# Kernel optimization log

Measured on AMD Instinct MI355X. Metric: run time of the kernel, lower is better.

## Reference

```python
import jax, jax.numpy as jnp
import numpy as np

KSIZE = 7
CUBIC_A = -0.5


def cubic_contribution(x, a=CUBIC_A):
    ax = jnp.abs(x)
    ax2 = ax * ax
    ax3 = ax * ax2
    cont_01 = ((a + 2) * ax3 - (a + 3) * ax2 + 1) * (ax <= 1).astype(x.dtype)
    cont_12 = (a * ax3 - 5 * a * ax2 + 8 * a * ax - 4 * a) * jnp.logical_and(ax > 1, ax <= 2).astype(x.dtype)
    return cont_01 + cont_12


def projective_grid(H, W, m, eps_x=0.0, eps_y=0.0):
    # Apply 3x3 homography m to pixel centers (x+eps_x, y+eps_y); returns (2, H*W).
    xs = jnp.arange(W, dtype=jnp.float32) + eps_x
    ys = jnp.arange(H, dtype=jnp.float32) + eps_y
    yy, xx = jnp.meshgrid(ys, xs, indexing='ij')
    xx = xx.ravel()
    yy = yy.ravel()
    X = m[0, 0] * xx + m[0, 1] * yy + m[0, 2]
    Y = m[1, 0] * xx + m[1, 1] * yy + m[1, 2]
    Z = m[2, 0] * xx + m[2, 1] * yy + m[2, 2]
    return jnp.stack((X / Z, Y / Z))


def setup_inputs() -> dict:
    key = jax.random.key(0)
    k1, k2 = jax.random.split(key)
    H = W = 1024
    N = H * W
    # near-identity homography (avoids degenerate perspective divide)
    m_inverse = jnp.eye(3, dtype=jnp.float32) + 0.001 * jax.random.normal(k1, (3, 3), dtype=jnp.float32)
    # source-space sampling positions, in-image range
    grid = jax.random.uniform(k2, (2, N), dtype=jnp.float32) * jnp.array([[W - 1.0], [H - 1.0]], dtype=jnp.float32)
    yi = jnp.arange(N, dtype=jnp.int32)
    return {"m_inverse": m_inverse, "grid": grid, "H": H, "W": W, "yi": yi}


def reference(m_inverse, grid, H, W, yi):
    K = KSIZE
    pad = K // 2
    offset = (K % 2) / 2  # 0.5 for odd kernels

    pos = grid + 1 - offset                      # (2, N)
    pos_frac = pos - jnp.floor(pos)              # (2, N)

    pl = projective_grid(H, W, m_inverse, eps_x=-0.5)
    pr = projective_grid(H, W, m_inverse, eps_x=0.5)
    pt = projective_grid(H, W, m_inverse, eps_y=-0.5)
    pb = projective_grid(H, W, m_inverse, eps_y=0.5)

    du = (pb - pt)[:, yi][:, :, None, None]      # (2, N, 1, 1)
    dv = (pr - pl)[:, yi][:, :, None, None]      # (2, N, 1, 1)

    # regularize |du| >= 1
    len_du = jnp.sqrt(du[0] ** 2 + du[1] ** 2)   # (N, 1, 1)
    mask_du = len_du < 1.0
    du = jnp.where(mask_du[None], du / len_du[None], du)
    len_du = jnp.where(mask_du, 1.0, len_du)

    # regularize |dv| >= 1
    len_dv = jnp.sqrt(dv[0] ** 2 + dv[1] ** 2)
    mask_dv = len_dv < 1.0
    dv = jnp.where(mask_dv[None], dv / len_dv[None], dv)
    len_dv = jnp.where(mask_dv, 1.0, len_dv)

    det = du[0] * dv[1] - du[1] * dv[0]          # (N, 1, 1)
    len_du = len_du * det
    len_dv = len_dv * det

    pos_w = jnp.linspace(pad - K + 1, pad, K).astype(jnp.float32) + offset  # (K,)
    pw = pos_frac[:, :, None] - pos_w[None, None, :]                        # (2, N, K)
    pos_wx = pw[0][:, None, :]                   # (N, 1, K)
    pos_wy = pw[1][:, :, None]                   # (N, K, 1)

    pos_wxp = (dv[1] * pos_wx - du[1] * pos_wy) / len_du  # (N, K, K)
    pos_wyp = (du[0] * pos_wy - dv[0] * pos_wx) / len_dv  # (N, K, K)

    x = du[0] * pos_wxp + du[1] * pos_wyp        # (N, K, K)
    y = dv[0] * pos_wxp + dv[1] * pos_wyp        # (N, K, K)

    weight = (cubic_contribution(x) * cubic_contribution(y)).reshape(x.shape[0], -1)  # (N, K*K)
    weight = weight / jnp.sum(weight, axis=-1, keepdims=True)
    return weight
```

## Files before the change

### kernel.cpp

```cpp
#include <hip/hip_runtime.h>

#define K 7
#define KK 49
#define BLK 256

__device__ __forceinline__ float cubic_c(float x) {
    float ax  = __builtin_fabsf(x);
    float ax2 = ax * ax;
    float ax3 = ax2 * ax;
    float c01 =  1.5f * ax3 - 2.5f * ax2 + 1.0f;
    float c12 = -0.5f * ax3 + 2.5f * ax2 - 4.0f * ax + 2.0f;
    return (ax <= 1.0f) ? c01 : ((ax <= 2.0f) ? c12 : 0.0f);
}

__global__ __launch_bounds__(BLK) void kest_kernel(
    const float* __restrict__ m,
    const float* __restrict__ grid,
    const int*   __restrict__ Wp,
    const int*   __restrict__ yi,
    float*       __restrict__ out,
    int N)
{
    __shared__ float sw[KK][BLK + 1];
    __shared__ float srs[BLK];

    const int tid = threadIdx.x;
    const int i   = blockIdx.x * BLK + tid;

    const float m00 = m[0], m01 = m[1], m02 = m[2];
    const float m10 = m[3], m11 = m[4], m12 = m[5];
    const float m20 = m[6], m21 = m[7], m22 = m[8];
    const int   W   = Wp[0];

    if (i < N) {
        const int j = yi[i];
        const float xx = (float)(j % W);
        const float yy = (float)(j / W);

        const float X0 = m00 * xx + m01 * yy + m02;
        const float Y0 = m10 * xx + m11 * yy + m12;
        const float Z0 = m20 * xx + m21 * yy + m22;

        const float izy = 1.0f / (Z0 * Z0 - 0.25f * m21 * m21);
        float du0 = (m01 * Z0 - m21 * X0) * izy;
        float du1 = (m11 * Z0 - m21 * Y0) * izy;
        const float izx = 1.0f / (Z0 * Z0 - 0.25f * m20 * m20);
        float dv0 = (m00 * Z0 - m20 * X0) * izx;
        float dv1 = (m10 * Z0 - m20 * Y0) * izx;

        float len_du = __builtin_sqrtf(du0 * du0 + du1 * du1);
        if (len_du < 1.0f) {
            float r = 1.0f / len_du;
            du0 *= r; du1 *= r;
            len_du = 1.0f;
        }
        float len_dv = __builtin_sqrtf(dv0 * dv0 + dv1 * dv1);
        if (len_dv < 1.0f) {
            float r = 1.0f / len_dv;
            dv0 *= r; dv1 *= r;
            len_dv = 1.0f;
        }

        const float det  = du0 * dv1 - du1 * dv0;
        const float r_du = 1.0f / (len_du * det);
        const float r_dv = 1.0f / (len_dv * det);

        const float px = grid[i]     + 0.5f;
        const float py = grid[N + i] + 0.5f;
        const float fx = px - __builtin_floorf(px);
        const float fy = py - __builtin_floorf(py);

        float wsum = 0.0f;
#pragma unroll
        for (int ky = 0; ky < K; ++ky) {
            const float wyv = fy + 2.5f - (float)ky;
#pragma unroll
            for (int kx = 0; kx < K; ++kx) {
                const float wxv = fx + 2.5f - (float)kx;
                const float a = (dv1 * wxv - du1 * wyv) * r_du;
                const float b = (du0 * wyv - dv0 * wxv) * r_dv;
                const float x = du0 * a + du1 * b;
                const float y = dv0 * a + dv1 * b;
                const float wv = cubic_c(x) * cubic_c(y);
                sw[ky * K + kx][tid] = wv;
                wsum += wv;
            }
        }
        srs[tid] = 1.0f / wsum;
    }
    __syncthreads();

    const long long base  = (long long)blockIdx.x * (BLK * KK);
    const long long limit = (long long)N * KK;
#pragma unroll
    for (int t = 0; t < KK; ++t) {
        const int idx = t * BLK + tid;
        const int p   = idx / KK;
        const int q   = idx - p * KK;
        const long long g = base + idx;
        if (g < limit) out[g] = sw[q][p] * srs[p];
    }
}

extern "C" void kernel_launch(void* const* d_in, const int* in_sizes, int n_in,
                              void* d_out, int out_size, void* d_ws, size_t ws_size,
                              hipStream_t stream) {
    const float* m    = (const float*)d_in[0];
    const float* grid = (const float*)d_in[1];
    const int*   Wp   = (const int*)d_in[3];
    const int*   yi   = (const int*)d_in[4];
    float*       out  = (float*)d_out;
    const int N = in_sizes[4];

    const int blocks = (N + BLK - 1) / BLK;
    kest_kernel<<<blocks, BLK, 0, stream>>>(m, grid, Wp, yi, out, N);
}
```

Measured before the change: 254.7 us.

## Halve LDS staging, vectorize output stores, fold inner transform into 2x2 matrix

Weights are now held in registers and written to a half-sized shared buffer in two rounds of 128 pixels each. Each round is stored to global memory as float4. The per-tap affine transform is precomputed as a 2x2 matrix, so each tap costs two FMAs, and the cubic kernel is rewritten without branches using max/fma. The smaller LDS footprint and the launch-bounds occupancy hint aim to raise occupancy and widen stores. The cost is 49 live registers per thread and an extra barrier round. The float4 tail guard assumes N*KK is divisible by 4.

```diff
diff --git a/kernel.cpp b/kernel.cpp
--- a/kernel.cpp
+++ b/kernel.cpp
@@ -3,17 +3,19 @@
 #define K 7
 #define KK 49
 #define BLK 256
+#define HALF_PIX 128
+#define CHUNK_FLOATS (HALF_PIX * KK)
+#define CHUNK_F4 (CHUNK_FLOATS / 4)
 
 __device__ __forceinline__ float cubic_c(float x) {
-    float ax  = __builtin_fabsf(x);
-    float ax2 = ax * ax;
-    float ax3 = ax2 * ax;
-    float c01 =  1.5f * ax3 - 2.5f * ax2 + 1.0f;
-    float c12 = -0.5f * ax3 + 2.5f * ax2 - 4.0f * ax + 2.0f;
-    return (ax <= 1.0f) ? c01 : ((ax <= 2.0f) ? c12 : 0.0f);
+    float ax = __builtin_fabsf(x);
+    float t2 = __builtin_fmaxf(2.0f - ax, 0.0f);
+    float t1 = __builtin_fmaxf(1.0f - ax, 0.0f);
+    float r  = (t2 * t2) * __builtin_fmaf(0.5f, t2, -0.5f);
+    return __builtin_fmaf(t1 * t1, __builtin_fmaf(-2.0f, t1, 1.0f), r);
 }
 
-__global__ __launch_bounds__(BLK) void kest_kernel(
+__global__ __launch_bounds__(BLK, 5) void kest_kernel(
     const float* __restrict__ m,
     const float* __restrict__ grid,
     const int*   __restrict__ Wp,
@@ -21,18 +23,21 @@
     float*       __restrict__ out,
     int N)
 {
-    __shared__ float sw[KK][BLK + 1];
-    __shared__ float srs[BLK];
+    __shared__ __align__(16) float lds[CHUNK_FLOATS];
 
     const int tid = threadIdx.x;
     const int i   = blockIdx.x * BLK + tid;
+    const bool valid = (i < N);
 
     const float m00 = m[0], m01 = m[1], m02 = m[2];
     const float m10 = m[3], m11 = m[4], m12 = m[5];
     const float m20 = m[6], m21 = m[7], m22 = m[8];
     const int   W   = Wp[0];
 
-    if (i < N) {
+    float w[KK];
+    float rs = 0.0f;
+
+    if (valid) {
         const int j = yi[i];
         const float xx = (float)(j % W);
         const float yy = (float)(j / W);
@@ -65,6 +70,11 @@
         const float r_du = 1.0f / (len_du * det);
         const float r_dv = 1.0f / (len_dv * det);
 
+        const float Axx = du0 * dv1 * r_du - du1 * dv0 * r_dv;
+        const float Axy = du0 * du1 * (r_dv - r_du);
+        const float Ayx = dv0 * dv1 * (r_du - r_dv);
+        const float Ayy = du0 * dv1 * r_dv - du1 * dv0 * r_du;
+
         const float px = grid[i]     + 0.5f;
         const float py = grid[N + i] + 0.5f;
         const float fx = px - __builtin_floorf(px);
@@ -74,31 +84,55 @@
 #pragma unroll
         for (int ky = 0; ky < K; ++ky) {
             const float wyv = fy + 2.5f - (float)ky;
+            const float xk  = Axy * wyv;
+            const float yk  = Ayy * wyv;
 #pragma unroll
             for (int kx = 0; kx < K; ++kx) {
                 const float wxv = fx + 2.5f - (float)kx;
-                const float a = (dv1 * wxv - du1 * wyv) * r_du;
-                const float b = (du0 * wyv - dv0 * wxv) * r_dv;
-                const float x = du0 * a + du1 * b;
-                const float y = dv0 * a + dv1 * b;
+                const float x = __builtin_fmaf(Axx, wxv, xk);
+                const float y = __builtin_fmaf(Ayx, wxv, yk);
                 const float wv = cubic_c(x) * cubic_c(y);
-                sw[ky * K + kx][tid] = wv;
+                w[ky * K + kx] = wv;
                 wsum += wv;
             }
         }
-        srs[tid] = 1.0f / wsum;
+        rs = 1.0f / wsum;
+    }
+
+    const long long blockBaseF = (long long)blockIdx.x * (BLK * KK);
+    const long long limitF4    = ((long long)N * KK) >> 2;
+
+    if (valid && tid < HALF_PIX) {
+        float* p = &lds[tid * KK];
+#pragma unroll
+        for (int q = 0; q < KK; ++q) p[q] = w[q] * rs;
+    }
+    __syncthreads();
+    {
+        const float4* src = (const float4*)lds;
+        float4*       dst = (float4*)(out + blockBaseF);
+        const long long g0 = blockBaseF >> 2;
+#pragma unroll
+        for (int t = tid; t < CHUNK_F4; t += BLK) {
+            if (g0 + t < limitF4) dst[t] = src[t];
+        }
     }
     __syncthreads();
 
-    const long long base  = (long long)blockIdx.x * (BLK * KK);
-    const long long limit = (long long)N * KK;
+    if (valid && tid >= HALF_PIX) {
+        float* p = &lds[(tid - HALF_PIX) * KK];
 #pragma unroll
-    for (int t = 0; t < KK; ++t) {
-        const int idx = t * BLK + tid;
-        const int p   = idx / KK;
-        const int q   = idx - p * KK;
-        const long long g = base + idx;
-        if (g < limit) out[g] = sw[q][p] * srs[p];
+        for (int q = 0; q < KK; ++q) p[q] = w[q] * rs;
+    }
+    __syncthreads();
+    {
+        const float4* src = (const float4*)lds;
+        float4*       dst = (float4*)(out + blockBaseF + CHUNK_FLOATS);
+        const long long g0 = (blockBaseF + CHUNK_FLOATS) >> 2;
+#pragma unroll
+        for (int t = tid; t < CHUNK_F4; t += BLK) {
+            if (g0 + t < limitF4) dst[t] = src[t];
+        }
     }
 }
 
```

New measurement: 217.7 us. -14.5%, faster.

## Split each pixel's 49 weights across four threads with vectorized float4 stores

Applied to the files above, without the earlier changes.

Each pixel's 7x7 weight computation is now spread over four lanes, which reduce the weight sum with shuffles and write normalized weights into a compact LDS tile that is copied out with float4 stores. The per-tap math is collapsed into a precomputed 2x2 linear map, and the cubic kernel is rewritten branch-free using clamped polynomials. W decoding uses shifts when W is a power of two. This raises parallelism and cuts registers per thread, aiming for better occupancy and wider global stores. It costs four times as many blocks and some redundant per-pixel setup on each lane.

```diff
diff --git a/kernel.cpp b/kernel.cpp
--- a/kernel.cpp
+++ b/kernel.cpp
@@ -3,17 +3,20 @@
 #define K 7
 #define KK 49
 #define BLK 256
+#define TPP 4
+#define PPB (BLK / TPP)
+#define NW 13
+#define CHUNK_F4 (PPB * KK / 4)
 
 __device__ __forceinline__ float cubic_c(float x) {
-    float ax  = __builtin_fabsf(x);
-    float ax2 = ax * ax;
-    float ax3 = ax2 * ax;
-    float c01 =  1.5f * ax3 - 2.5f * ax2 + 1.0f;
-    float c12 = -0.5f * ax3 + 2.5f * ax2 - 4.0f * ax + 2.0f;
-    return (ax <= 1.0f) ? c01 : ((ax <= 2.0f) ? c12 : 0.0f);
+    float ax = __builtin_fabsf(x);
+    float t2 = __builtin_fmaxf(2.0f - ax, 0.0f);
+    float t1 = __builtin_fmaxf(1.0f - ax, 0.0f);
+    float r  = (t2 * t2) * __builtin_fmaf(0.5f, t2, -0.5f);
+    return __builtin_fmaf(t1 * t1, __builtin_fmaf(-2.0f, t1, 1.0f), r);
 }
 
-__global__ __launch_bounds__(BLK) void kest_kernel(
+__global__ __launch_bounds__(BLK, 8) void kest_kernel(
     const float* __restrict__ m,
     const float* __restrict__ grid,
     const int*   __restrict__ Wp,
@@ -21,11 +24,12 @@
     float*       __restrict__ out,
     int N)
 {
-    __shared__ float sw[KK][BLK + 1];
-    __shared__ float srs[BLK];
+    __shared__ __align__(16) float lds[PPB * KK];
 
-    const int tid = threadIdx.x;
-    const int i   = blockIdx.x * BLK + tid;
+    const int tid  = threadIdx.x;
+    const int sub  = tid & (TPP - 1);
+    const int pixL = tid >> 2;
+    const int i    = blockIdx.x * PPB + pixL;
 
     const float m00 = m[0], m01 = m[1], m02 = m[2];
     const float m10 = m[3], m11 = m[4], m12 = m[5];
@@ -34,8 +38,16 @@
 
     if (i < N) {
         const int j = yi[i];
-        const float xx = (float)(j % W);
-        const float yy = (float)(j / W);
+        int yyI, xxI;
+        if ((W & (W - 1)) == 0) {
+            yyI = j >> (__ffs(W) - 1);
+            xxI = j & (W - 1);
+        } else {
+            yyI = j / W;
+            xxI = j - yyI * W;
+        }
+        const float xx = (float)xxI;
+        const float yy = (float)yyI;
 
         const float X0 = m00 * xx + m01 * yy + m02;
         const float Y0 = m10 * xx + m11 * yy + m12;
@@ -65,40 +77,54 @@
         const float r_du = 1.0f / (len_du * det);
         const float r_dv = 1.0f / (len_dv * det);
 
-        const float px = grid[i]     + 0.5f;
-        const float py = grid[N + i] + 0.5f;
-        const float fx = px - __builtin_floorf(px);
-        const float fy = py - __builtin_floorf(py);
+        const float p1 = du0 * dv1, p2 = du1 * dv0;
+        const float Axx = p1 * r_du - p2 * r_dv;
+        const float Axy = du0 * du1 * (r_dv - r_du);
+        const float Ayx = dv0 * dv1 * (r_du - r_dv);
+        const float Ayy = p1 * r_dv - p2 * r_du;
 
+        const float px  = grid[i]     + 0.5f;
+        const float py  = grid[N + i] + 0.5f;
+        const float fxc = (px - __builtin_floorf(px)) + 2.5f;
+        const float fyc = (py - __builtin_floorf(py)) + 2.5f;
+
+        float wv[NW];
         float wsum = 0.0f;
+        int kx = sub, ky = 0;
 #pragma unroll
-        for (int ky = 0; ky < K; ++ky) {
-            const float wyv = fy + 2.5f - (float)ky;
+        for (int qq = 0; qq < NW; ++qq) {
+            const float wxv = fxc - (float)kx;
+            const float wyv = fyc - (float)ky;
+            const float x = __builtin_fmaf(Axx, wxv, Axy * wyv);
+            const float y = __builtin_fmaf(Ayx, wxv, Ayy * wyv);
+            float t = cubic_c(x) * cubic_c(y);
+            if (qq == NW - 1 && sub >= 1) t = 0.0f;
+            wv[qq] = t;
+            wsum += t;
+            kx += TPP;
+            if (kx >= K) { kx -= K; ++ky; }
+        }
+        wsum += __shfl_xor(wsum, 1);
+        wsum += __shfl_xor(wsum, 2);
+        const float rs = 1.0f / wsum;
+
+        float* p = &lds[pixL * KK + sub];
 #pragma unroll
-            for (int kx = 0; kx < K; ++kx) {
-                const float wxv = fx + 2.5f - (float)kx;
-                const float a = (dv1 * wxv - du1 * wyv) * r_du;
-                const float b = (du0 * wyv - dv0 * wxv) * r_dv;
-                const float x = du0 * a + du1 * b;
-                const float y = dv0 * a + dv1 * b;
-                const float wv = cubic_c(x) * cubic_c(y);
-                sw[ky * K + kx][tid] = wv;
-                wsum += wv;
-            }
+        for (int qq = 0; qq < NW; ++qq) {
+            if (qq < NW - 1 || sub == 0)
+                p[4 * qq] = wv[qq] * rs;
         }
-        srs[tid] = 1.0f / wsum;
     }
     __syncthreads();
 
-    const long long base  = (long long)blockIdx.x * (BLK * KK);
-    const long long limit = (long long)N * KK;
+    const long long baseF4 = (long long)blockIdx.x * CHUNK_F4;
+    const long long limF4  = ((long long)N * KK) >> 2;
+    const float4* src = (const float4*)lds;
+    float4*       dst = (float4*)out + baseF4;
 #pragma unroll
-    for (int t = 0; t < KK; ++t) {
-        const int idx = t * BLK + tid;
-        const int p   = idx / KK;
-        const int q   = idx - p * KK;
-        const long long g = base + idx;
-        if (g < limit) out[g] = sw[q][p] * srs[p];
+    for (int k = 0; k < 4; ++k) {
+        const int t = tid + k * BLK;
+        if (t < CHUNK_F4 && baseF4 + t < limF4) dst[t] = src[t];
     }
 }
 
@@ -112,6 +138,6 @@
     float*       out  = (float*)d_out;
     const int N = in_sizes[4];
 
-    const int blocks = (N + BLK - 1) / BLK;
+    const int blocks = (N + PPB - 1) / PPB;
     kest_kernel<<<blocks, BLK, 0, stream>>>(m, grid, Wp, yi, out, N);
 }
```

Result: faster. 244.0 us (-4.2%).
